# Kernel optimization log

Hardware: AMD Instinct MI355X
Metric: run time of the kernel (lower is better)

The kernel has to match this reference:

```python
import jax, jax.numpy as jnp
import numpy as np

# Config (matches init_kwargs)
N, P, K, DIMS = 16, 1024, 16, 3
C_IN, C_MID, C_OUT, DM = 64, 64, 128, 4
C_CAT = C_MID + C_IN          # channels entering depthwise-separable conv
KK = K * K
BN_EPS = 1e-5


def setup_inputs() -> dict:
    key = jax.random.key(0)
    ks = jax.random.split(key, 24)
    s = 0.05  # small init scale for weights
    inp = {
        # forward args
        "rep_pt": jax.random.normal(ks[0], (N, P, DIMS), jnp.float32),
        "pts":    jax.random.normal(ks[1], (N, P, K, DIMS), jnp.float32),
        "fts":    jax.random.normal(ks[2], (N, P, K, C_IN), jnp.float32),
        # dense1 / dense2 (point lifting MLP), weights stored (in, out)
        "w1": jax.random.normal(ks[3], (DIMS, C_MID), jnp.float32) * s,
        "b1": jnp.zeros((C_MID,), jnp.float32),
        "w2": jax.random.normal(ks[4], (C_MID, C_MID), jnp.float32) * s,
        "b2": jnp.zeros((C_MID,), jnp.float32),
        # conv1: Conv2d(dims, K*K, (1,K)); weight (KK, dims, K)
        "wc1": jax.random.normal(ks[5], (KK, DIMS, K), jnp.float32) * s,
        "bc1": jnp.zeros((KK,), jnp.float32),
        # x_dense1 (ELU) and x_dense2 (no activation)
        "wx1": jax.random.normal(ks[6], (KK, KK), jnp.float32) * s,
        "bx1": jnp.zeros((KK,), jnp.float32),
        "wx2": jax.random.normal(ks[7], (KK, KK), jnp.float32) * s,
        "bx2": jnp.zeros((KK,), jnp.float32),
        # depthwise Conv2d(C_CAT, C_CAT*DM, (1,K), groups=C_CAT): weight (C_CAT, DM, K)
        "wdw": jax.random.normal(ks[8], (C_CAT, DM, K), jnp.float32) * s,
        "bdw": jnp.zeros((C_CAT * DM,), jnp.float32),
        # pointwise Conv2d(C_CAT*DM, C_OUT, 1): weight stored (C_CAT*DM, C_OUT)
        "wpw": jax.random.normal(ks[9], (C_CAT * DM, C_OUT), jnp.float32) * s,
        "bpw": jnp.zeros((C_OUT,), jnp.float32),
        # BatchNorm2d(C_OUT) in eval mode (running stats)
        "bn_gamma": jnp.ones((C_OUT,), jnp.float32),
        "bn_beta":  jnp.zeros((C_OUT,), jnp.float32),
        "bn_mean":  jax.random.normal(ks[10], (C_OUT,), jnp.float32) * 0.1,
        "bn_var":   jax.random.uniform(ks[11], (C_OUT,), jnp.float32, 0.5, 1.5),
    }
    return inp


def reference(rep_pt, pts, fts, w1, b1, w2, b2, wc1, bc1, wx1, bx1, wx2, bx2,
              wdw, bdw, wpw, bpw, bn_gamma, bn_beta, bn_mean, bn_var):
    elu = jax.nn.elu
    n, p, k = pts.shape[0], pts.shape[1], pts.shape[2]

    # localize points around representative point: (N,P,K,dims)
    pts_local = pts - rep_pt[:, :, None, :]

    # lift coordinates to C_mid features (two Dense+ELU)
    h = elu(pts_local @ w1 + b1)
    h = elu(h @ w2 + b2)
    fts_cat = jnp.concatenate([h, fts], axis=-1)  # (N,P,K,C_CAT)

    # learned X-transform: conv1 over the K neighbors -> (N,P,K*K)
    X = elu(jnp.einsum('npkd,odk->npo', pts_local, wc1) + bc1)
    X = elu(X @ wx1 + bx1)
    X = X @ wx2 + bx2            # x_dense2: no activation
    X = X.reshape(n, p, k, k)    # (N,P,K,K)

    # apply X-transform to concatenated features
    fts_X = jnp.einsum('npij,npjc->npic', X, fts_cat)  # (N,P,K,C_CAT)

    # depthwise conv (kernel (1,K), groups=C_CAT, depth multiplier DM)
    # torch grouped-conv channel order: out channel o = c*DM + d
    dw = jnp.einsum('npkc,cdk->npcd', fts_X, wdw).reshape(n, p, -1) + bdw
    # pointwise 1x1 conv -> C_OUT, then ELU
    y = elu(dw @ wpw + bpw)      # (N,P,C_OUT)
    # BatchNorm2d in eval mode (per-channel affine with running stats)
    y = (y - bn_mean) * (bn_gamma / jnp.sqrt(bn_var + BN_EPS)) + bn_beta
    return y                     # (N,P,C_OUT)
```

## Files before the change

kernel.cpp:

```cpp
#include <hip/hip_runtime.h>

#define NPTS 16384
#define MPB  16
#define NTHR 256
#define WS_NEEDED 401408u

typedef __attribute__((ext_vector_type(8))) short bf16x8;
typedef __attribute__((ext_vector_type(4))) float f32x4;

__device__ __forceinline__ unsigned short f2bf(float x) {
    unsigned u = __float_as_uint(x);
    return (unsigned short)((u + 0x7FFFu + ((u >> 16) & 1u)) >> 16);
}
__device__ __forceinline__ unsigned pk2(float a, float b) {
    return (unsigned)f2bf(a) | ((unsigned)f2bf(b) << 16);
}
__device__ __forceinline__ float bf2f(unsigned short h) {
    return __uint_as_float(((unsigned)h) << 16);
}
__device__ __forceinline__ float elu_f(float x) {
    return x > 0.f ? x : (__expf(x) - 1.f);
}

__device__ __forceinline__ bf16x8 load_bfrag(const float* __restrict__ W, int N,
                                             int kt, int nt, int lane) {
    int k0  = kt * 32 + ((lane >> 4) << 3);
    int col = nt * 16 + (lane & 15);
    const float* s = W + k0 * N + col;
    bf16x8 r;
#pragma unroll
    for (int j = 0; j < 8; j++) r[j] = (short)f2bf(s[j * N]);
    return r;
}

__global__ void pack_weights(const float* __restrict__ w2,
                             const float* __restrict__ wx1,
                             const float* __restrict__ wx2,
                             const float* __restrict__ wpw,
                             unsigned short* __restrict__ dst) {
    int gid  = blockIdx.x * 256 + threadIdx.x;
    int frag = gid >> 6, lane = gid & 63;
    const float* src; int N, fl;
    if      (frag <   8) { src = w2;  N =  64; fl = frag;       }
    else if (frag < 136) { src = wx1; N = 256; fl = frag - 8;   }
    else if (frag < 264) { src = wx2; N = 256; fl = frag - 136; }
    else                 { src = wpw; N = 128; fl = frag - 264; }
    int NT  = N >> 4;
    int kt  = fl / NT, nt = fl - kt * NT;
    int k0  = kt * 32 + (lane >> 4) * 8;
    int col = nt * 16 + (lane & 15);
    const float* s = src + k0 * N + col;
    unsigned v[4];
#pragma unroll
    for (int u = 0; u < 4; u++) {
        unsigned lo = f2bf(s[(2 * u) * N]);
        unsigned hi = f2bf(s[(2 * u + 1) * N]);
        v[u] = lo | (hi << 16);
    }
    *(uint4*)&dst[gid * 8] = make_uint4(v[0], v[1], v[2], v[3]);
}

template <bool PACKED>
__global__ __launch_bounds__(NTHR, 2)
void xconv_main(const float* __restrict__ rep_pt, const float* __restrict__ pts,
                const float* __restrict__ fts,
                const float* __restrict__ w1,  const float* __restrict__ b1,
                const float* __restrict__ w2,  const float* __restrict__ b2,
                const float* __restrict__ wc1, const float* __restrict__ bc1,
                const float* __restrict__ wx1, const float* __restrict__ bx1,
                const float* __restrict__ wx2, const float* __restrict__ bx2,
                const float* __restrict__ wdw, const float* __restrict__ bdw,
                const float* __restrict__ wpw, const float* __restrict__ bpw,
                const float* __restrict__ bn_gamma, const float* __restrict__ bn_beta,
                const float* __restrict__ bn_mean,  const float* __restrict__ bn_var,
                const unsigned short* __restrict__ wpack,
                float* __restrict__ out) {
    __shared__ __align__(16) char smem[60928];
    float*          s_ptsl = (float*)smem;
    unsigned short* s_h2f  = (unsigned short*)(smem + 3072);
    unsigned short* s_h1   = (unsigned short*)(smem + 35840);
    unsigned short* s_x0   = (unsigned short*)(smem + 35840);
    unsigned short* s_x2f  = (unsigned short*)(smem + 35840);
    unsigned short* s_x1   = (unsigned short*)(smem + 44288);
    unsigned short* s_dw   = (unsigned short*)(smem + 44288);

    const int t    = threadIdx.x;
    const int lane = t & 63;
    const int w    = t >> 6;
    const int cl   = lane & 15;
    const int hh   = lane >> 4;
    const int gp0  = blockIdx.x * MPB;

    for (int idx = t; idx < MPB * 48; idx += NTHR) {
        int m = idx / 48, r = idx - m * 48;
        int k = r / 3,    d = r - k * 3;
        int gp = gp0 + m;
        s_ptsl[idx] = pts[(gp * 16 + k) * 3 + d] - rep_pt[gp * 3 + d];
    }
    __syncthreads();

    {
        const bf16x8* wp = (const bf16x8*)wpack;
        bf16x8 Bf[8];
#pragma unroll
        for (int f = 0; f < 8; f++) {
            if (PACKED) Bf[f] = wp[f * 64 + lane];
            else        Bf[f] = load_bfrag(w2, 64, f >> 2, f & 3, lane);
        }
        float bias[4];
#pragma unroll
        for (int nt = 0; nt < 4; nt++) bias[nt] = b2[nt * 16 + cl];

        for (int R = 0; R < 2; R++) {
            {
                int lr  = t >> 1;
                int row = 128 * R + lr;
                int m = row >> 4, k = row & 15;
                float p0 = s_ptsl[m * 48 + k * 3 + 0];
                float p1 = s_ptsl[m * 48 + k * 3 + 1];
                float p2 = s_ptsl[m * 48 + k * 3 + 2];
                int cb = (t & 1) * 32;
#pragma unroll
                for (int cc = 0; cc < 4; cc++) {
                    unsigned v[4];
#pragma unroll
                    for (int u = 0; u < 4; u++) {
                        int c0 = cb + cc * 8 + u * 2;
                        float a  = fmaf(p0, w1[c0],     fmaf(p1, w1[64 + c0],     fmaf(p2, w1[128 + c0],     b1[c0])));
                        float bb = fmaf(p0, w1[c0 + 1], fmaf(p1, w1[64 + c0 + 1], fmaf(p2, w1[128 + c0 + 1], b1[c0 + 1])));
                        v[u] = pk2(elu_f(a), elu_f(bb));
                    }
                    *(uint4*)&s_h1[lr * 72 + cb + cc * 8] = make_uint4(v[0], v[1], v[2], v[3]);
                }
            }
            __syncthreads();
            {
#pragma unroll
                for (int i = 0; i < 2; i++) {
                    int rtl = w * 2 + i;
                    int m   = 8 * R + rtl;
                    bf16x8 a0 = *(const bf16x8*)&s_h1[(rtl * 16 + cl) * 72 + 0  + hh * 8];
                    bf16x8 a1 = *(const bf16x8*)&s_h1[(rtl * 16 + cl) * 72 + 32 + hh * 8];
#pragma unroll
                    for (int nt = 0; nt < 4; nt++) {
                        f32x4 acc = {bias[nt], bias[nt], bias[nt], bias[nt]};
                        acc = __builtin_amdgcn_mfma_f32_16x16x32_bf16(a0, Bf[0 * 4 + nt], acc, 0, 0, 0);
                        acc = __builtin_amdgcn_mfma_f32_16x16x32_bf16(a1, Bf[1 * 4 + nt], acc, 0, 0, 0);
                        unsigned lo = pk2(elu_f(acc[0]), elu_f(acc[1]));
                        unsigned hi = pk2(elu_f(acc[2]), elu_f(acc[3]));
                        unsigned short* dp = &s_h2f[(((m * 4 + nt) * 32) + (hh >> 1) * 16 + cl) * 8 + (hh & 1) * 4];
                        *(uint2*)dp = make_uint2(lo, hi);
                    }
                }
            }
            __syncthreads();
        }
    }

    {
        float wreg[48];
#pragma unroll
        for (int q = 0; q < 12; q++) {
            float4 wv = *(const float4*)&wc1[t * 48 + q * 4];
            wreg[q * 4 + 0] = wv.x; wreg[q * 4 + 1] = wv.y;
            wreg[q * 4 + 2] = wv.z; wreg[q * 4 + 3] = wv.w;
        }
        float bo = bc1[t];
#pragma unroll 1
        for (int m = 0; m < MPB; m++) {
            float acc = bo;
#pragma unroll
            for (int q = 0; q < 12; q++) {
                float4 pv = *(const float4*)&s_ptsl[m * 48 + q * 4];
                acc = fmaf(pv.x, wreg[((q * 4 + 0) % 3) * 16 + (q * 4 + 0) / 3], acc);
                acc = fmaf(pv.y, wreg[((q * 4 + 1) % 3) * 16 + (q * 4 + 1) / 3], acc);
                acc = fmaf(pv.z, wreg[((q * 4 + 2) % 3) * 16 + (q * 4 + 2) / 3], acc);
                acc = fmaf(pv.w, wreg[((q * 4 + 3) % 3) * 16 + (q * 4 + 3) / 3], acc);
            }
            s_x0[m * 264 + t] = f2bf(elu_f(acc));
        }
    }
    __syncthreads();

    {
        const bf16x8* wp = (const bf16x8*)wpack + 512;
        f32x4 acc[4];
#pragma unroll
        for (int q = 0; q < 4; q++) {
            float bv = bx1[(w * 4 + q) * 16 + cl];
            acc[q] = (f32x4){bv, bv, bv, bv};
        }
#pragma unroll
        for (int kt = 0; kt < 8; kt++) {
            bf16x8 a = *(const bf16x8*)&s_x0[cl * 264 + kt * 32 + hh * 8];
#pragma unroll
            for (int q = 0; q < 4; q++) {
                int nt = w * 4 + q;
                bf16x8 b;
                if (PACKED) b = wp[(kt * 16 + nt) * 64 + lane];
                else        b = load_bfrag(wx1, 256, kt, nt, lane);
                acc[q] = __builtin_amdgcn_mfma_f32_16x16x32_bf16(a, b, acc[q], 0, 0, 0);
            }
        }
#pragma unroll
        for (int q = 0; q < 4; q++) {
            int nt = w * 4 + q;
#pragma unroll
            for (int r = 0; r < 4; r++) {
                int m = hh * 4 + r;
                s_x1[m * 264 + nt * 16 + cl] = f2bf(elu_f(acc[q][r]));
            }
        }
    }
    __syncthreads();

    {
        const bf16x8* wp = (const bf16x8*)wpack + 8704;
        f32x4 acc[4];
#pragma unroll
        for (int q = 0; q < 4; q++) {
            float bv = bx2[(w * 4 + q) * 16 + cl];
            acc[q] = (f32x4){bv, bv, bv, bv};
        }
#pragma unroll
        for (int kt = 0; kt < 8; kt++) {
            bf16x8 a = *(const bf16x8*)&s_x1[cl * 264 + kt * 32 + hh * 8];
#pragma unroll
            for (int q = 0; q < 4; q++) {
                int nt = w * 4 + q;
                bf16x8 b;
                if (PACKED) b = wp[(kt * 16 + nt) * 64 + lane];
                else        b = load_bfrag(wx2, 256, kt, nt, lane);
                acc[q] = __builtin_amdgcn_mfma_f32_16x16x32_bf16(a, b, acc[q], 0, 0, 0);
            }
        }
#pragma unroll
        for (int q = 0; q < 4; q++) {
            int ntE = w * 4 + q;
            int lp  = (cl >> 3) * 16 + ntE;
            int jj  = cl & 7;
#pragma unroll
            for (int r = 0; r < 4; r++) {
                int m = hh * 4 + r;
                s_x2f[(m * 32 + lp) * 8 + jj] = f2bf(acc[q][r]);
            }
        }
    }
    __syncthreads();

    {
        const int cA = w * 16 + cl;
        const int cB = 64 + w * 16 + cl;
        float wdA[16], wdB[16];
#pragma unroll
        for (int d = 0; d < 4; d++) {
            float4 va = *(const float4*)&wdw[cA * 64 + d * 16 + 4 * hh];
            wdA[d * 4 + 0] = va.x; wdA[d * 4 + 1] = va.y; wdA[d * 4 + 2] = va.z; wdA[d * 4 + 3] = va.w;
            float4 vb = *(const float4*)&wdw[cB * 64 + d * 16 + 4 * hh];
            wdB[d * 4 + 0] = vb.x; wdB[d * 4 + 1] = vb.y; wdB[d * 4 + 2] = vb.z; wdB[d * 4 + 3] = vb.w;
        }
        float4 bdA = *(const float4*)&bdw[cA * 4];
        float4 bdB = *(const float4*)&bdw[cB * 4];
        const float* ftsp = fts + (size_t)gp0 * 1024 + (w * 16 + cl);

        float f0[8], f1[8];
        auto LDF = [&](int m, float* f) {
            if (lane < 32) {
                const float* p = ftsp + (m * 16 + hh * 8) * 64;
#pragma unroll
                for (int j = 0; j < 8; j++) f[j] = p[j * 64];
            }
        };
        auto BODY = [&](int m, float* fc_, float* fn_) {
            if (m < 15) LDF(m + 1, fn_);
            bf16x8 a  = {};
            bf16x8 bh = {};
            if (lane < 32) {
                a  = *(const bf16x8*)&s_x2f[(m * 32 + lane) * 8];
                bh = *(const bf16x8*)&s_h2f[((m * 4 + w) * 32 + lane) * 8];
            }
            f32x4 accA = {0.f, 0.f, 0.f, 0.f};
            f32x4 accB = {0.f, 0.f, 0.f, 0.f};
            accA = __builtin_amdgcn_mfma_f32_16x16x32_bf16(a, bh, accA, 0, 0, 0);
            bf16x8 bf_ = {};
            if (lane < 32) {
                union { bf16x8 v; uint4 u; } ub;
                ub.u = make_uint4(pk2(fc_[0], fc_[1]), pk2(fc_[2], fc_[3]),
                                  pk2(fc_[4], fc_[5]), pk2(fc_[6], fc_[7]));
                bf_ = ub.v;
            }
            accB = __builtin_amdgcn_mfma_f32_16x16x32_bf16(a, bf_, accB, 0, 0, 0);
            float oA[4], oB[4];
#pragma unroll
            for (int d = 0; d < 4; d++) {
                float sA = accA[0] * wdA[d * 4 + 0];
                sA = fmaf(accA[1], wdA[d * 4 + 1], sA);
                sA = fmaf(accA[2], wdA[d * 4 + 2], sA);
                sA = fmaf(accA[3], wdA[d * 4 + 3], sA);
                sA += __shfl_xor(sA, 16);
                sA += __shfl_xor(sA, 32);
                oA[d] = sA;
                float sB = accB[0] * wdB[d * 4 + 0];
                sB = fmaf(accB[1], wdB[d * 4 + 1], sB);
                sB = fmaf(accB[2], wdB[d * 4 + 2], sB);
                sB = fmaf(accB[3], wdB[d * 4 + 3], sB);
                sB += __shfl_xor(sB, 16);
                sB += __shfl_xor(sB, 32);
                oB[d] = sB;
            }
            if (hh == 0) {
                ushort4 va, vb;
                va.x = f2bf(oA[0] + bdA.x); va.y = f2bf(oA[1] + bdA.y);
                va.z = f2bf(oA[2] + bdA.z); va.w = f2bf(oA[3] + bdA.w);
                vb.x = f2bf(oB[0] + bdB.x); vb.y = f2bf(oB[1] + bdB.y);
                vb.z = f2bf(oB[2] + bdB.z); vb.w = f2bf(oB[3] + bdB.w);
                *(ushort4*)&s_dw[m * 520 + cA * 4] = va;
                *(ushort4*)&s_dw[m * 520 + cB * 4] = vb;
            }
        };
        LDF(0, f0);
#pragma unroll
        for (int mm = 0; mm < 8; mm++) {
            BODY(2 * mm + 0, f0, f1);
            BODY(2 * mm + 1, f1, f0);
        }
    }
    __syncthreads();

    {
        const bf16x8* wp = (const bf16x8*)wpack + 16896;
        f32x4 acc[2];
#pragma unroll
        for (int q = 0; q < 2; q++) {
            float bv = bpw[(w * 2 + q) * 16 + cl];
            acc[q] = (f32x4){bv, bv, bv, bv};
        }
#pragma unroll
        for (int kt = 0; kt < 16; kt++) {
            bf16x8 a = *(const bf16x8*)&s_dw[cl * 520 + kt * 32 + hh * 8];
#pragma unroll
            for (int q = 0; q < 2; q++) {
                int nt = w * 2 + q;
                bf16x8 b;
                if (PACKED) b = wp[(kt * 8 + nt) * 64 + lane];
                else        b = load_bfrag(wpw, 128, kt, nt, lane);
                acc[q] = __builtin_amdgcn_mfma_f32_16x16x32_bf16(a, b, acc[q], 0, 0, 0);
            }
        }
#pragma unroll
        for (int q = 0; q < 2; q++) {
            int co = (w * 2 + q) * 16 + cl;
            float scale = bn_gamma[co] * rsqrtf(bn_var[co] + 1e-5f);
            float shift = bn_beta[co] - bn_mean[co] * scale;
#pragma unroll
            for (int r = 0; r < 4; r++) {
                int m = hh * 4 + r;
                out[(gp0 + m) * 128 + co] = fmaf(elu_f(acc[q][r]), scale, shift);
            }
        }
    }
}

extern "C" void kernel_launch(void* const* d_in, const int* in_sizes, int n_in,
                              void* d_out, int out_size, void* d_ws, size_t ws_size,
                              hipStream_t stream) {
    const float* rep_pt   = (const float*)d_in[0];
    const float* pts      = (const float*)d_in[1];
    const float* fts      = (const float*)d_in[2];
    const float* w1       = (const float*)d_in[3];
    const float* b1       = (const float*)d_in[4];
    const float* w2       = (const float*)d_in[5];
    const float* b2       = (const float*)d_in[6];
    const float* wc1      = (const float*)d_in[7];
    const float* bc1      = (const float*)d_in[8];
    const float* wx1      = (const float*)d_in[9];
    const float* bx1      = (const float*)d_in[10];
    const float* wx2      = (const float*)d_in[11];
    const float* bx2      = (const float*)d_in[12];
    const float* wdw      = (const float*)d_in[13];
    const float* bdw      = (const float*)d_in[14];
    const float* wpw      = (const float*)d_in[15];
    const float* bpw      = (const float*)d_in[16];
    const float* bn_gamma = (const float*)d_in[17];
    const float* bn_beta  = (const float*)d_in[18];
    const float* bn_mean  = (const float*)d_in[19];
    const float* bn_var   = (const float*)d_in[20];
    float* out = (float*)d_out;

    const bool packed = (d_ws != nullptr) && (ws_size >= (size_t)WS_NEEDED);
    unsigned short* wpack = (unsigned short*)d_ws;

    if (packed) {
        pack_weights<<<98, 256, 0, stream>>>(w2, wx1, wx2, wpw, wpack);
        xconv_main<true><<<NPTS / MPB, NTHR, 0, stream>>>(
            rep_pt, pts, fts, w1, b1, w2, b2, wc1, bc1, wx1, bx1, wx2, bx2,
            wdw, bdw, wpw, bpw, bn_gamma, bn_beta, bn_mean, bn_var, wpack, out);
    } else {
        xconv_main<false><<<NPTS / MPB, NTHR, 0, stream>>>(
            rep_pt, pts, fts, w1, b1, w2, b2, wc1, bc1, wx1, bx1, wx2, bx2,
            wdw, bdw, wpw, bpw, bn_gamma, bn_beta, bn_mean, bn_var, (const unsigned short*)nullptr, out);
    }
}
```

Before: 198.7 us.

## Double block to 512 threads and split per-stage work across eight waves

Raises the block size from 256 to 512 threads, which means eight waves instead of four, with launch bounds set to 4. Each stage's work is repartitioned to match: the h2 MFMA handles one row tile per wave, conv1 splits the points in half, the X-dense and pointwise GEMMs give each wave half as many N tiles, and the depthwise stage splits the h-branch and the fts-branch across the wave halves. The aim is more latency hiding and wave-level parallelism per block within the same shared memory. In exchange, register budgets get tighter, and some threads sit idle in the h1 stage.

```diff
diff --git a/kernel.cpp b/kernel.cpp
--- a/kernel.cpp
+++ b/kernel.cpp
@@ -2,7 +2,7 @@
 
 #define NPTS 16384
 #define MPB  16
-#define NTHR 256
+#define NTHR 512
 #define WS_NEEDED 401408u
 
 typedef __attribute__((ext_vector_type(8))) short bf16x8;
@@ -61,7 +61,7 @@
 }
 
 template <bool PACKED>
-__global__ __launch_bounds__(NTHR, 2)
+__global__ __launch_bounds__(NTHR, 4)
 void xconv_main(const float* __restrict__ rep_pt, const float* __restrict__ pts,
                 const float* __restrict__ fts,
                 const float* __restrict__ w1,  const float* __restrict__ b1,
@@ -112,7 +112,7 @@
         for (int nt = 0; nt < 4; nt++) bias[nt] = b2[nt * 16 + cl];
 
         for (int R = 0; R < 2; R++) {
-            {
+            if (t < 256) {
                 int lr  = t >> 1;
                 int row = 128 * R + lr;
                 int m = row >> 4, k = row & 15;
@@ -135,22 +135,19 @@
             }
             __syncthreads();
             {
-#pragma unroll
-                for (int i = 0; i < 2; i++) {
-                    int rtl = w * 2 + i;
-                    int m   = 8 * R + rtl;
-                    bf16x8 a0 = *(const bf16x8*)&s_h1[(rtl * 16 + cl) * 72 + 0  + hh * 8];
-                    bf16x8 a1 = *(const bf16x8*)&s_h1[(rtl * 16 + cl) * 72 + 32 + hh * 8];
-#pragma unroll
-                    for (int nt = 0; nt < 4; nt++) {
-                        f32x4 acc = {bias[nt], bias[nt], bias[nt], bias[nt]};
-                        acc = __builtin_amdgcn_mfma_f32_16x16x32_bf16(a0, Bf[0 * 4 + nt], acc, 0, 0, 0);
-                        acc = __builtin_amdgcn_mfma_f32_16x16x32_bf16(a1, Bf[1 * 4 + nt], acc, 0, 0, 0);
-                        unsigned lo = pk2(elu_f(acc[0]), elu_f(acc[1]));
-                        unsigned hi = pk2(elu_f(acc[2]), elu_f(acc[3]));
-                        unsigned short* dp = &s_h2f[(((m * 4 + nt) * 32) + (hh >> 1) * 16 + cl) * 8 + (hh & 1) * 4];
-                        *(uint2*)dp = make_uint2(lo, hi);
-                    }
+                int rtl = w;
+                int m   = 8 * R + rtl;
+                bf16x8 a0 = *(const bf16x8*)&s_h1[(rtl * 16 + cl) * 72 + 0  + hh * 8];
+                bf16x8 a1 = *(const bf16x8*)&s_h1[(rtl * 16 + cl) * 72 + 32 + hh * 8];
+#pragma unroll
+                for (int nt = 0; nt < 4; nt++) {
+                    f32x4 acc = {bias[nt], bias[nt], bias[nt], bias[nt]};
+                    acc = __builtin_amdgcn_mfma_f32_16x16x32_bf16(a0, Bf[0 * 4 + nt], acc, 0, 0, 0);
+                    acc = __builtin_amdgcn_mfma_f32_16x16x32_bf16(a1, Bf[1 * 4 + nt], acc, 0, 0, 0);
+                    unsigned lo = pk2(elu_f(acc[0]), elu_f(acc[1]));
+                    unsigned hi = pk2(elu_f(acc[2]), elu_f(acc[3]));
+                    unsigned short* dp = &s_h2f[(((m * 4 + nt) * 32) + (hh >> 1) * 16 + cl) * 8 + (hh & 1) * 4];
+                    *(uint2*)dp = make_uint2(lo, hi);
                 }
             }
             __syncthreads();
@@ -158,16 +155,19 @@
     }
 
     {
+        const int o     = t & 255;
+        const int mbase = (t >> 8) * 8;
         float wreg[48];
 #pragma unroll
         for (int q = 0; q < 12; q++) {
-            float4 wv = *(const float4*)&wc1[t * 48 + q * 4];
+            float4 wv = *(const float4*)&wc1[o * 48 + q * 4];
             wreg[q * 4 + 0] = wv.x; wreg[q * 4 + 1] = wv.y;
             wreg[q * 4 + 2] = wv.z; wreg[q * 4 + 3] = wv.w;
         }
-        float bo = bc1[t];
+        float bo = bc1[o];
 #pragma unroll 1
-        for (int m = 0; m < MPB; m++) {
+        for (int ml = 0; ml < 8; ml++) {
+            int m = mbase + ml;
             float acc = bo;
 #pragma unroll
             for (int q = 0; q < 12; q++) {
@@ -177,25 +177,25 @@
                 acc = fmaf(pv.z, wreg[((q * 4 + 2) % 3) * 16 + (q * 4 + 2) / 3], acc);
                 acc = fmaf(pv.w, wreg[((q * 4 + 3) % 3) * 16 + (q * 4 + 3) / 3], acc);
             }
-            s_x0[m * 264 + t] = f2bf(elu_f(acc));
+            s_x0[m * 264 + o] = f2bf(elu_f(acc));
         }
     }
     __syncthreads();
 
     {
         const bf16x8* wp = (const bf16x8*)wpack + 512;
-        f32x4 acc[4];
-#pragma unroll
-        for (int q = 0; q < 4; q++) {
-            float bv = bx1[(w * 4 + q) * 16 + cl];
+        f32x4 acc[2];
+#pragma unroll
+        for (int q = 0; q < 2; q++) {
+            float bv = bx1[(w * 2 + q) * 16 + cl];
             acc[q] = (f32x4){bv, bv, bv, bv};
         }
 #pragma unroll
         for (int kt = 0; kt < 8; kt++) {
             bf16x8 a = *(const bf16x8*)&s_x0[cl * 264 + kt * 32 + hh * 8];
 #pragma unroll
-            for (int q = 0; q < 4; q++) {
-                int nt = w * 4 + q;
+            for (int q = 0; q < 2; q++) {
+                int nt = w * 2 + q;
                 bf16x8 b;
                 if (PACKED) b = wp[(kt * 16 + nt) * 64 + lane];
                 else        b = load_bfrag(wx1, 256, kt, nt, lane);
@@ -203,8 +203,8 @@
             }
         }
 #pragma unroll
-        for (int q = 0; q < 4; q++) {
-            int nt = w * 4 + q;
+        for (int q = 0; q < 2; q++) {
+            int nt = w * 2 + q;
 #pragma unroll
             for (int r = 0; r < 4; r++) {
                 int m = hh * 4 + r;
@@ -216,18 +216,18 @@
 
     {
         const bf16x8* wp = (const bf16x8*)wpack + 8704;
-        f32x4 acc[4];
-#pragma unroll
-        for (int q = 0; q < 4; q++) {
-            float bv = bx2[(w * 4 + q) * 16 + cl];
+        f32x4 acc[2];
+#pragma unroll
+        for (int q = 0; q < 2; q++) {
+            float bv = bx2[(w * 2 + q) * 16 + cl];
             acc[q] = (f32x4){bv, bv, bv, bv};
         }
 #pragma unroll
         for (int kt = 0; kt < 8; kt++) {
             bf16x8 a = *(const bf16x8*)&s_x1[cl * 264 + kt * 32 + hh * 8];
 #pragma unroll
-            for (int q = 0; q < 4; q++) {
-                int nt = w * 4 + q;
+            for (int q = 0; q < 2; q++) {
+                int nt = w * 2 + q;
                 bf16x8 b;
                 if (PACKED) b = wp[(kt * 16 + nt) * 64 + lane];
                 else        b = load_bfrag(wx2, 256, kt, nt, lane);
@@ -235,8 +235,8 @@
             }
         }
 #pragma unroll
-        for (int q = 0; q < 4; q++) {
-            int ntE = w * 4 + q;
+        for (int q = 0; q < 2; q++) {
+            int ntE = w * 2 + q;
             int lp  = (cl >> 3) * 16 + ntE;
             int jj  = cl & 7;
 #pragma unroll
@@ -249,23 +249,22 @@
     __syncthreads();
 
     {
-        const int cA = w * 16 + cl;
-        const int cB = 64 + w * 16 + cl;
-        float wdA[16], wdB[16];
+        const int  cH    = (w & 3) * 16 + cl;
+        const bool isF   = (w >= 4);
+        const int  cFull = isF ? (64 + cH) : cH;
+        float wd[16];
 #pragma unroll
         for (int d = 0; d < 4; d++) {
-            float4 va = *(const float4*)&wdw[cA * 64 + d * 16 + 4 * hh];
-            wdA[d * 4 + 0] = va.x; wdA[d * 4 + 1] = va.y; wdA[d * 4 + 2] = va.z; wdA[d * 4 + 3] = va.w;
-            float4 vb = *(const float4*)&wdw[cB * 64 + d * 16 + 4 * hh];
-            wdB[d * 4 + 0] = vb.x; wdB[d * 4 + 1] = vb.y; wdB[d * 4 + 2] = vb.z; wdB[d * 4 + 3] = vb.w;
-        }
-        float4 bdA = *(const float4*)&bdw[cA * 4];
-        float4 bdB = *(const float4*)&bdw[cB * 4];
-        const float* ftsp = fts + (size_t)gp0 * 1024 + (w * 16 + cl);
+            float4 v = *(const float4*)&wdw[cFull * 64 + d * 16 + 4 * hh];
+            wd[d * 4 + 0] = v.x; wd[d * 4 + 1] = v.y;
+            wd[d * 4 + 2] = v.z; wd[d * 4 + 3] = v.w;
+        }
+        float4 bd = *(const float4*)&bdw[cFull * 4];
+        const float* ftsp = fts + (size_t)gp0 * 1024 + cH;
 
         float f0[8], f1[8];
         auto LDF = [&](int m, float* f) {
-            if (lane < 32) {
+            if (isF && lane < 32) {
                 const float* p = ftsp + (m * 16 + hh * 8) * 64;
 #pragma unroll
                 for (int j = 0; j < 8; j++) f[j] = p[j * 64];
@@ -273,49 +272,37 @@
         };
         auto BODY = [&](int m, float* fc_, float* fn_) {
             if (m < 15) LDF(m + 1, fn_);
-            bf16x8 a  = {};
-            bf16x8 bh = {};
-            if (lane < 32) {
-                a  = *(const bf16x8*)&s_x2f[(m * 32 + lane) * 8];
-                bh = *(const bf16x8*)&s_h2f[((m * 4 + w) * 32 + lane) * 8];
-            }
-            f32x4 accA = {0.f, 0.f, 0.f, 0.f};
-            f32x4 accB = {0.f, 0.f, 0.f, 0.f};
-            accA = __builtin_amdgcn_mfma_f32_16x16x32_bf16(a, bh, accA, 0, 0, 0);
-            bf16x8 bf_ = {};
-            if (lane < 32) {
-                union { bf16x8 v; uint4 u; } ub;
-                ub.u = make_uint4(pk2(fc_[0], fc_[1]), pk2(fc_[2], fc_[3]),
-                                  pk2(fc_[4], fc_[5]), pk2(fc_[6], fc_[7]));
-                bf_ = ub.v;
-            }
-            accB = __builtin_amdgcn_mfma_f32_16x16x32_bf16(a, bf_, accB, 0, 0, 0);
-            float oA[4], oB[4];
+            bf16x8 a = {};
+            if (lane < 32) a = *(const bf16x8*)&s_x2f[(m * 32 + lane) * 8];
+            bf16x8 b = {};
+            if (isF) {
+                if (lane < 32) {
+                    union { bf16x8 v; uint4 u; } ub;
+                    ub.u = make_uint4(pk2(fc_[0], fc_[1]), pk2(fc_[2], fc_[3]),
+                                      pk2(fc_[4], fc_[5]), pk2(fc_[6], fc_[7]));
+                    b = ub.v;
+                }
+            } else {
+                if (lane < 32) b = *(const bf16x8*)&s_h2f[((m * 4 + (w & 3)) * 32 + lane) * 8];
+            }
+            f32x4 acc = {0.f, 0.f, 0.f, 0.f};
+            acc = __builtin_amdgcn_mfma_f32_16x16x32_bf16(a, b, acc, 0, 0, 0);
+            float o[4];
 #pragma unroll
             for (int d = 0; d < 4; d++) {
-                float sA = accA[0] * wdA[d * 4 + 0];
-                sA = fmaf(accA[1], wdA[d * 4 + 1], sA);
-                sA = fmaf(accA[2], wdA[d * 4 + 2], sA);
-                sA = fmaf(accA[3], wdA[d * 4 + 3], sA);
-                sA += __shfl_xor(sA, 16);
-                sA += __shfl_xor(sA, 32);
-                oA[d] = sA;
-                float sB = accB[0] * wdB[d * 4 + 0];
-                sB = fmaf(accB[1], wdB[d * 4 + 1], sB);
-                sB = fmaf(accB[2], wdB[d * 4 + 2], sB);
-                sB = fmaf(accB[3], wdB[d * 4 + 3], sB);
-                sB += __shfl_xor(sB, 16);
-                sB += __shfl_xor(sB, 32);
-                oB[d] = sB;
+                float s = acc[0] * wd[d * 4 + 0];
+                s = fmaf(acc[1], wd[d * 4 + 1], s);
+                s = fmaf(acc[2], wd[d * 4 + 2], s);
+                s = fmaf(acc[3], wd[d * 4 + 3], s);
+                s += __shfl_xor(s, 16);
+                s += __shfl_xor(s, 32);
+                o[d] = s;
             }
             if (hh == 0) {
-                ushort4 va, vb;
-                va.x = f2bf(oA[0] + bdA.x); va.y = f2bf(oA[1] + bdA.y);
-                va.z = f2bf(oA[2] + bdA.z); va.w = f2bf(oA[3] + bdA.w);
-                vb.x = f2bf(oB[0] + bdB.x); vb.y = f2bf(oB[1] + bdB.y);
-                vb.z = f2bf(oB[2] + bdB.z); vb.w = f2bf(oB[3] + bdB.w);
-                *(ushort4*)&s_dw[m * 520 + cA * 4] = va;
-                *(ushort4*)&s_dw[m * 520 + cB * 4] = vb;
+                ushort4 v;
+                v.x = f2bf(o[0] + bd.x); v.y = f2bf(o[1] + bd.y);
+                v.z = f2bf(o[2] + bd.z); v.w = f2bf(o[3] + bd.w);
+                *(ushort4*)&s_dw[m * 520 + cFull * 4] = v;
             }
         };
         LDF(0, f0);
@@ -329,34 +316,23 @@
 
     {
         const bf16x8* wp = (const bf16x8*)wpack + 16896;
-        f32x4 acc[2];
-#pragma unroll
-        for (int q = 0; q < 2; q++) {
-            float bv = bpw[(w * 2 + q) * 16 + cl];
-            acc[q] = (f32x4){bv, bv, bv, bv};
-        }
+        float bv = bpw[w * 16 + cl];
+        f32x4 acc = {bv, bv, bv, bv};
 #pragma unroll
         for (int kt = 0; kt < 16; kt++) {
             bf16x8 a = *(const bf16x8*)&s_dw[cl * 520 + kt * 32 + hh * 8];
-#pragma unroll
-            for (int q = 0; q < 2; q++) {
-                int nt = w * 2 + q;
-                bf16x8 b;
-                if (PACKED) b = wp[(kt * 8 + nt) * 64 + lane];
-                else        b = load_bfrag(wpw, 128, kt, nt, lane);
-                acc[q] = __builtin_amdgcn_mfma_f32_16x16x32_bf16(a, b, acc[q], 0, 0, 0);
-            }
-        }
-#pragma unroll
-        for (int q = 0; q < 2; q++) {
-            int co = (w * 2 + q) * 16 + cl;
-            float scale = bn_gamma[co] * rsqrtf(bn_var[co] + 1e-5f);
-            float shift = bn_beta[co] - bn_mean[co] * scale;
-#pragma unroll
-            for (int r = 0; r < 4; r++) {
-                int m = hh * 4 + r;
-                out[(gp0 + m) * 128 + co] = fmaf(elu_f(acc[q][r]), scale, shift);
-            }
+            bf16x8 b;
+            if (PACKED) b = wp[(kt * 8 + w) * 64 + lane];
+            else        b = load_bfrag(wpw, 128, kt, w, lane);
+            acc = __builtin_amdgcn_mfma_f32_16x16x32_bf16(a, b, acc, 0, 0, 0);
+        }
+        int co = w * 16 + cl;
+        float scale = bn_gamma[co] * rsqrtf(bn_var[co] + 1e-5f);
+        float shift = bn_beta[co] - bn_mean[co] * scale;
+#pragma unroll
+        for (int r = 0; r < 4; r++) {
+            int m = hh * 4 + r;
+            out[(gp0 + m) * 128 + co] = fmaf(elu_f(acc[r]), scale, shift);
         }
     }
 }
```

Result: no change. 200.9 us (+1.1%).

## Split fused X-conv kernel into prep and main kernels via workspace intermediates

Applied to the files above, without the earlier changes.

The single fused kernel is split in two. The first kernel computes the lifted point features (h2) and the X-transform matrix with 32 points per 512-thread block and writes both as bf16 to the workspace. The second kernel reads them, runs the X-transform, depthwise and pointwise stages at higher occupancy, and software-prefetches the next point's operands. The aim is to cut per-block register and LDS pressure and raise occupancy, at the cost of an extra global round trip of about 42 MB and one more launch; the split path is taken only when the workspace is large enough.

```diff
diff --git a/kernel.cpp b/kernel.cpp
--- a/kernel.cpp
+++ b/kernel.cpp
@@ -1,9 +1,13 @@
 #include <hip/hip_runtime.h>
 
 #define NPTS 16384
-#define MPB  16
 #define NTHR 256
-#define WS_NEEDED 401408u
+#define MPREP 32
+
+#define WS_PACK   401408u
+#define OFF_X2    401408u
+#define OFF_H2    8790016u
+#define WS_FULL   42344448u
 
 typedef __attribute__((ext_vector_type(8))) short bf16x8;
 typedef __attribute__((ext_vector_type(4))) float f32x4;
@@ -60,21 +64,334 @@
     *(uint4*)&dst[gid * 8] = make_uint4(v[0], v[1], v[2], v[3]);
 }
 
+__global__ __launch_bounds__(512, 4)
+void xprep(const float* __restrict__ rep_pt, const float* __restrict__ pts,
+           const float* __restrict__ w1,  const float* __restrict__ b1,
+           const float* __restrict__ b2,
+           const float* __restrict__ wc1, const float* __restrict__ bc1,
+           const float* __restrict__ bx1, const float* __restrict__ bx2,
+           const unsigned short* __restrict__ wpack,
+           unsigned short* __restrict__ gH2, unsigned short* __restrict__ gX2) {
+    __shared__ __align__(16) char smem[43008];
+    float*          s_ptsl = (float*)smem;
+    unsigned short* s_h1   = (unsigned short*)(smem + 6144);
+    unsigned short* s_x0   = (unsigned short*)(smem + 6144);
+    unsigned short* s_x1   = (unsigned short*)(smem + 23040);
+
+    const int t    = threadIdx.x;
+    const int lane = t & 63;
+    const int w    = t >> 6;
+    const int cl   = lane & 15;
+    const int hh   = lane >> 4;
+    const int gp0  = blockIdx.x * MPREP;
+
+    for (int idx = t; idx < MPREP * 48; idx += 512) {
+        int m = idx / 48, r = idx - m * 48;
+        int k = r / 3,    d = r - k * 3;
+        int gp = gp0 + m;
+        s_ptsl[idx] = pts[(gp * 16 + k) * 3 + d] - rep_pt[gp * 3 + d];
+    }
+    __syncthreads();
+
+    {
+        const bf16x8* wp = (const bf16x8*)wpack;
+        bf16x8 Bf[8];
+#pragma unroll
+        for (int f = 0; f < 8; f++) Bf[f] = wp[f * 64 + lane];
+        float bias[4];
+#pragma unroll
+        for (int nt = 0; nt < 4; nt++) bias[nt] = b2[nt * 16 + cl];
+
+        for (int R = 0; R < 2; R++) {
+            {
+                int lr  = t >> 1;
+                int row = 256 * R + lr;
+                int m = row >> 4, k = row & 15;
+                float p0 = s_ptsl[m * 48 + k * 3 + 0];
+                float p1 = s_ptsl[m * 48 + k * 3 + 1];
+                float p2 = s_ptsl[m * 48 + k * 3 + 2];
+                int cb = (t & 1) * 32;
+#pragma unroll
+                for (int cc = 0; cc < 4; cc++) {
+                    unsigned v[4];
+#pragma unroll
+                    for (int u = 0; u < 4; u++) {
+                        int c0 = cb + cc * 8 + u * 2;
+                        float a  = fmaf(p0, w1[c0],     fmaf(p1, w1[64 + c0],     fmaf(p2, w1[128 + c0],     b1[c0])));
+                        float bb = fmaf(p0, w1[c0 + 1], fmaf(p1, w1[64 + c0 + 1], fmaf(p2, w1[128 + c0 + 1], b1[c0 + 1])));
+                        v[u] = pk2(elu_f(a), elu_f(bb));
+                    }
+                    *(uint4*)&s_h1[lr * 72 + cb + cc * 8] = make_uint4(v[0], v[1], v[2], v[3]);
+                }
+            }
+            __syncthreads();
+            {
+#pragma unroll
+                for (int i = 0; i < 2; i++) {
+                    int rtl  = w * 2 + i;
+                    int mloc = R * 16 + rtl;
+                    size_t gp = (size_t)(gp0 + mloc);
+                    bf16x8 a0 = *(const bf16x8*)&s_h1[(rtl * 16 + cl) * 72 + 0  + hh * 8];
+                    bf16x8 a1 = *(const bf16x8*)&s_h1[(rtl * 16 + cl) * 72 + 32 + hh * 8];
+#pragma unroll
+                    for (int nt = 0; nt < 4; nt++) {
+                        f32x4 acc = {bias[nt], bias[nt], bias[nt], bias[nt]};
+                        acc = __builtin_amdgcn_mfma_f32_16x16x32_bf16(a0, Bf[0 * 4 + nt], acc, 0, 0, 0);
+                        acc = __builtin_amdgcn_mfma_f32_16x16x32_bf16(a1, Bf[1 * 4 + nt], acc, 0, 0, 0);
+                        unsigned lo = pk2(elu_f(acc[0]), elu_f(acc[1]));
+                        unsigned hi = pk2(elu_f(acc[2]), elu_f(acc[3]));
+                        unsigned short* dp = &gH2[((gp * 4 + nt) * 32 + (hh >> 1) * 16 + cl) * 8 + (hh & 1) * 4];
+                        *(uint2*)dp = make_uint2(lo, hi);
+                    }
+                }
+            }
+            __syncthreads();
+        }
+    }
+
+    {
+        const int o  = t & 255;
+        const int mb = (t >> 8) * 16;
+        float wreg[48];
+#pragma unroll
+        for (int q = 0; q < 12; q++) {
+            float4 wv = *(const float4*)&wc1[o * 48 + q * 4];
+            wreg[q * 4 + 0] = wv.x; wreg[q * 4 + 1] = wv.y;
+            wreg[q * 4 + 2] = wv.z; wreg[q * 4 + 3] = wv.w;
+        }
+        float bo = bc1[o];
+#pragma unroll 1
+        for (int ml = 0; ml < 16; ml++) {
+            int m = mb + ml;
+            float acc = bo;
+#pragma unroll
+            for (int q = 0; q < 12; q++) {
+                float4 pv = *(const float4*)&s_ptsl[m * 48 + q * 4];
+                acc = fmaf(pv.x, wreg[((q * 4 + 0) % 3) * 16 + (q * 4 + 0) / 3], acc);
+                acc = fmaf(pv.y, wreg[((q * 4 + 1) % 3) * 16 + (q * 4 + 1) / 3], acc);
+                acc = fmaf(pv.z, wreg[((q * 4 + 2) % 3) * 16 + (q * 4 + 2) / 3], acc);
+                acc = fmaf(pv.w, wreg[((q * 4 + 3) % 3) * 16 + (q * 4 + 3) / 3], acc);
+            }
+            s_x0[m * 264 + o] = f2bf(elu_f(acc));
+        }
+    }
+    __syncthreads();
+
+    {
+        const bf16x8* wp = (const bf16x8*)wpack + 512;
+        f32x4 acc[2][2];
+#pragma unroll
+        for (int q = 0; q < 2; q++) {
+            float bv = bx1[(w * 2 + q) * 16 + cl];
+#pragma unroll
+            for (int mt = 0; mt < 2; mt++) acc[mt][q] = (f32x4){bv, bv, bv, bv};
+        }
+#pragma unroll
+        for (int kt = 0; kt < 8; kt++) {
+            bf16x8 b0 = wp[(kt * 16 + w * 2 + 0) * 64 + lane];
+            bf16x8 b1 = wp[(kt * 16 + w * 2 + 1) * 64 + lane];
+#pragma unroll
+            for (int mt = 0; mt < 2; mt++) {
+                bf16x8 a = *(const bf16x8*)&s_x0[(mt * 16 + cl) * 264 + kt * 32 + hh * 8];
+                acc[mt][0] = __builtin_amdgcn_mfma_f32_16x16x32_bf16(a, b0, acc[mt][0], 0, 0, 0);
+                acc[mt][1] = __builtin_amdgcn_mfma_f32_16x16x32_bf16(a, b1, acc[mt][1], 0, 0, 0);
+            }
+        }
+        __syncthreads();
+#pragma unroll
+        for (int q = 0; q < 2; q++) {
+            int nt = w * 2 + q;
+#pragma unroll
+            for (int mt = 0; mt < 2; mt++) {
+#pragma unroll
+                for (int r = 0; r < 4; r++) {
+                    int m = mt * 16 + hh * 4 + r;
+                    s_x1[m * 264 + nt * 16 + cl] = f2bf(elu_f(acc[mt][q][r]));
+                }
+            }
+        }
+    }
+    __syncthreads();
+
+    {
+        const bf16x8* wp = (const bf16x8*)wpack + 8704;
+        f32x4 acc[2][2];
+#pragma unroll
+        for (int q = 0; q < 2; q++) {
+            float bv = bx2[(w * 2 + q) * 16 + cl];
+#pragma unroll
+            for (int mt = 0; mt < 2; mt++) acc[mt][q] = (f32x4){bv, bv, bv, bv};
+        }
+#pragma unroll
+        for (int kt = 0; kt < 8; kt++) {
+            bf16x8 b0 = wp[(kt * 16 + w * 2 + 0) * 64 + lane];
+            bf16x8 b1 = wp[(kt * 16 + w * 2 + 1) * 64 + lane];
+#pragma unroll
+            for (int mt = 0; mt < 2; mt++) {
+                bf16x8 a = *(const bf16x8*)&s_x1[(mt * 16 + cl) * 264 + kt * 32 + hh * 8];
+                acc[mt][0] = __builtin_amdgcn_mfma_f32_16x16x32_bf16(a, b0, acc[mt][0], 0, 0, 0);
+                acc[mt][1] = __builtin_amdgcn_mfma_f32_16x16x32_bf16(a, b1, acc[mt][1], 0, 0, 0);
+            }
+        }
+#pragma unroll
+        for (int q = 0; q < 2; q++) {
+            int ntE = w * 2 + q;
+            int lp  = (cl >> 3) * 16 + ntE;
+            int jj  = cl & 7;
+#pragma unroll
+            for (int mt = 0; mt < 2; mt++) {
+#pragma unroll
+                for (int r = 0; r < 4; r++) {
+                    size_t gp = (size_t)(gp0 + mt * 16 + hh * 4 + r);
+                    gX2[gp * 256 + lp * 8 + jj] = f2bf(acc[mt][q][r]);
+                }
+            }
+        }
+    }
+}
+
+__global__ __launch_bounds__(NTHR, 4)
+void xmain(const float* __restrict__ fts,
+           const float* __restrict__ wdw, const float* __restrict__ bdw,
+           const float* __restrict__ bpw,
+           const float* __restrict__ bn_gamma, const float* __restrict__ bn_beta,
+           const float* __restrict__ bn_mean,  const float* __restrict__ bn_var,
+           const unsigned short* __restrict__ wpack,
+           const unsigned short* __restrict__ gH2,
+           const unsigned short* __restrict__ gX2,
+           float* __restrict__ out) {
+    __shared__ __align__(16) unsigned short s_dw[16 * 520];
+
+    const int t    = threadIdx.x;
+    const int lane = t & 63;
+    const int w    = t >> 6;
+    const int cl   = lane & 15;
+    const int hh   = lane >> 4;
+    const int gp0  = blockIdx.x * 16;
+
+    {
+        float wd[2][16];
+        float4 bd[2];
+#pragma unroll
+        for (int g = 0; g < 2; g++) {
+            int c = (w * 2 + g) * 16 + cl;
+#pragma unroll
+            for (int d = 0; d < 4; d++) {
+                float4 v = *(const float4*)&wdw[c * 64 + d * 16 + 4 * hh];
+                wd[g][d * 4 + 0] = v.x; wd[g][d * 4 + 1] = v.y;
+                wd[g][d * 4 + 2] = v.z; wd[g][d * 4 + 3] = v.w;
+            }
+            bd[g] = *(const float4*)&bdw[c * 4];
+        }
+
+        auto LOADA = [&](int m) -> bf16x8 {
+            bf16x8 a = {};
+            if (lane < 32) a = *(const bf16x8*)&gX2[(size_t)(gp0 + m) * 256 + lane * 8];
+            return a;
+        };
+        auto LOADB = [&](int m, int g) -> bf16x8 {
+            bf16x8 b = {};
+            int cg = w * 2 + g;
+            if (lane < 32) {
+                if (cg < 4) {
+                    b = *(const bf16x8*)&gH2[(((size_t)(gp0 + m) * 4 + cg) * 32 + lane) * 8];
+                } else {
+                    const float* p = fts + ((size_t)(gp0 + m) * 16 + hh * 8) * 64 + (cg - 4) * 16 + cl;
+                    union { bf16x8 v; uint4 u; } ub;
+                    ub.u = make_uint4(pk2(p[0],   p[64]),  pk2(p[128], p[192]),
+                                      pk2(p[256], p[320]), pk2(p[384], p[448]));
+                    b = ub.v;
+                }
+            }
+            return b;
+        };
+
+        bf16x8 a  = LOADA(0);
+        bf16x8 b0 = LOADB(0, 0);
+        bf16x8 b1 = LOADB(0, 1);
+#pragma unroll
+        for (int m = 0; m < 16; m++) {
+            bf16x8 na = {}, nb0 = {}, nb1 = {};
+            if (m < 15) {
+                na  = LOADA(m + 1);
+                nb0 = LOADB(m + 1, 0);
+                nb1 = LOADB(m + 1, 1);
+            }
+#pragma unroll
+            for (int g = 0; g < 2; g++) {
+                f32x4 acc = {0.f, 0.f, 0.f, 0.f};
+                acc = __builtin_amdgcn_mfma_f32_16x16x32_bf16(a, g ? b1 : b0, acc, 0, 0, 0);
+                float o[4];
+#pragma unroll
+                for (int d = 0; d < 4; d++) {
+                    float s = acc[0] * wd[g][d * 4 + 0];
+                    s = fmaf(acc[1], wd[g][d * 4 + 1], s);
+                    s = fmaf(acc[2], wd[g][d * 4 + 2], s);
+                    s = fmaf(acc[3], wd[g][d * 4 + 3], s);
+                    s += __shfl_xor(s, 16);
+                    s += __shfl_xor(s, 32);
+                    o[d] = s;
+                }
+                if (hh == 0) {
+                    int c = (w * 2 + g) * 16 + cl;
+                    float4 bdv = bd[g];
+                    ushort4 v;
+                    v.x = f2bf(o[0] + bdv.x); v.y = f2bf(o[1] + bdv.y);
+                    v.z = f2bf(o[2] + bdv.z); v.w = f2bf(o[3] + bdv.w);
+                    *(ushort4*)&s_dw[m * 520 + c * 4] = v;
+                }
+            }
+            a = na; b0 = nb0; b1 = nb1;
+        }
+    }
+    __syncthreads();
+
+    {
+        const bf16x8* wp = (const bf16x8*)wpack + 16896;
+        f32x4 acc[2];
+#pragma unroll
+        for (int q = 0; q < 2; q++) {
+            float bv = bpw[(w * 2 + q) * 16 + cl];
+            acc[q] = (f32x4){bv, bv, bv, bv};
+        }
+#pragma unroll
+        for (int kt = 0; kt < 16; kt++) {
+            bf16x8 a = *(const bf16x8*)&s_dw[cl * 520 + kt * 32 + hh * 8];
+#pragma unroll
+            for (int q = 0; q < 2; q++) {
+                bf16x8 b = wp[(kt * 8 + w * 2 + q) * 64 + lane];
+                acc[q] = __builtin_amdgcn_mfma_f32_16x16x32_bf16(a, b, acc[q], 0, 0, 0);
+            }
+        }
+#pragma unroll
+        for (int q = 0; q < 2; q++) {
+            int co = (w * 2 + q) * 16 + cl;
+            float scale = bn_gamma[co] * rsqrtf(bn_var[co] + 1e-5f);
+            float shift = bn_beta[co] - bn_mean[co] * scale;
+#pragma unroll
+            for (int r = 0; r < 4; r++) {
+                int m = hh * 4 + r;
+                out[(size_t)(gp0 + m) * 128 + co] = fmaf(elu_f(acc[q][r]), scale, shift);
+            }
+        }
+    }
+}
+
 template <bool PACKED>
 __global__ __launch_bounds__(NTHR, 2)
-void xconv_main(const float* __restrict__ rep_pt, const float* __restrict__ pts,
-                const float* __restrict__ fts,
-                const float* __restrict__ w1,  const float* __restrict__ b1,
-                const float* __restrict__ w2,  const float* __restrict__ b2,
-                const float* __restrict__ wc1, const float* __restrict__ bc1,
-                const float* __restrict__ wx1, const float* __restrict__ bx1,
-                const float* __restrict__ wx2, const float* __restrict__ bx2,
-                const float* __restrict__ wdw, const float* __restrict__ bdw,
-                const float* __restrict__ wpw, const float* __restrict__ bpw,
-                const float* __restrict__ bn_gamma, const float* __restrict__ bn_beta,
-                const float* __restrict__ bn_mean,  const float* __restrict__ bn_var,
-                const unsigned short* __restrict__ wpack,
-                float* __restrict__ out) {
+void xconv_fused(const float* __restrict__ rep_pt, const float* __restrict__ pts,
+                 const float* __restrict__ fts,
+                 const float* __restrict__ w1,  const float* __restrict__ b1,
+                 const float* __restrict__ w2,  const float* __restrict__ b2,
+                 const float* __restrict__ wc1, const float* __restrict__ bc1,
+                 const float* __restrict__ wx1, const float* __restrict__ bx1,
+                 const float* __restrict__ wx2, const float* __restrict__ bx2,
+                 const float* __restrict__ wdw, const float* __restrict__ bdw,
+                 const float* __restrict__ wpw, const float* __restrict__ bpw,
+                 const float* __restrict__ bn_gamma, const float* __restrict__ bn_beta,
+                 const float* __restrict__ bn_mean,  const float* __restrict__ bn_var,
+                 const unsigned short* __restrict__ wpack,
+                 float* __restrict__ out) {
     __shared__ __align__(16) char smem[60928];
     float*          s_ptsl = (float*)smem;
     unsigned short* s_h2f  = (unsigned short*)(smem + 3072);
@@ -89,9 +406,9 @@
     const int w    = t >> 6;
     const int cl   = lane & 15;
     const int hh   = lane >> 4;
-    const int gp0  = blockIdx.x * MPB;
-
-    for (int idx = t; idx < MPB * 48; idx += NTHR) {
+    const int gp0  = blockIdx.x * 16;
+
+    for (int idx = t; idx < 16 * 48; idx += NTHR) {
         int m = idx / 48, r = idx - m * 48;
         int k = r / 3,    d = r - k * 3;
         int gp = gp0 + m;
@@ -167,7 +484,7 @@
         }
         float bo = bc1[t];
 #pragma unroll 1
-        for (int m = 0; m < MPB; m++) {
+        for (int m = 0; m < 16; m++) {
             float acc = bo;
 #pragma unroll
             for (int q = 0; q < 12; q++) {
@@ -387,17 +704,26 @@
     const float* bn_var   = (const float*)d_in[20];
     float* out = (float*)d_out;
 
-    const bool packed = (d_ws != nullptr) && (ws_size >= (size_t)WS_NEEDED);
     unsigned short* wpack = (unsigned short*)d_ws;
 
-    if (packed) {
+    if (d_ws != nullptr && ws_size >= (size_t)WS_FULL) {
+        unsigned short* gX2 = (unsigned short*)((char*)d_ws + OFF_X2);
+        unsigned short* gH2 = (unsigned short*)((char*)d_ws + OFF_H2);
         pack_weights<<<98, 256, 0, stream>>>(w2, wx1, wx2, wpw, wpack);
-        xconv_main<true><<<NPTS / MPB, NTHR, 0, stream>>>(
+        xprep<<<NPTS / MPREP, 512, 0, stream>>>(
+            rep_pt, pts, w1, b1, b2, wc1, bc1, bx1, bx2, wpack, gH2, gX2);
+        xmain<<<NPTS / 16, NTHR, 0, stream>>>(
+            fts, wdw, bdw, bpw, bn_gamma, bn_beta, bn_mean, bn_var,
+            wpack, gH2, gX2, out);
+    } else if (d_ws != nullptr && ws_size >= (size_t)WS_PACK) {
+        pack_weights<<<98, 256, 0, stream>>>(w2, wx1, wx2, wpw, wpack);
+        xconv_fused<true><<<NPTS / 16, NTHR, 0, stream>>>(
             rep_pt, pts, fts, w1, b1, w2, b2, wc1, bc1, wx1, bx1, wx2, bx2,
             wdw, bdw, wpw, bpw, bn_gamma, bn_beta, bn_mean, bn_var, wpack, out);
     } else {
-        xconv_main<false><<<NPTS / MPB, NTHR, 0, stream>>>(
+        xconv_fused<false><<<NPTS / 16, NTHR, 0, stream>>>(
             rep_pt, pts, fts, w1, b1, w2, b2, wc1, bc1, wx1, bx1, wx2, bx2,
-            wdw, bdw, wpw, bpw, bn_gamma, bn_beta, bn_mean, bn_var, (const unsigned short*)nullptr, out);
-    }
-}
+            wdw, bdw, wpw, bpw, bn_gamma, bn_beta, bn_mean, bn_var,
+            (const unsigned short*)nullptr, out);
+    }
+}
```

Measured after the change: 235.1 us. 1.18x slower.
